# Performance work log

Hardware: AMD Instinct MI355X
Metric: run time of the kernel (lower is better)

The kernel has to match this reference:

```python
import jax, jax.numpy as jnp
import numpy as np

N, C, D = 16384, 1000, 512


def setup_inputs() -> dict:
    key = jax.random.key(0)
    k1, k2, k3 = jax.random.split(key, 3)
    features = jax.random.normal(k1, (N, D), dtype=jnp.float32)
    centers = jax.random.uniform(k2, (C, D), dtype=jnp.float32)  # torch.rand init
    labels = jax.random.randint(k3, (N,), 0, C, dtype=jnp.int64)
    return {"features": features, "centers": centers, "labels": labels}


def reference(features, centers, labels):
    # Full N x C squared Euclidean distance matrix (as in torch.cdist(...)**2)
    f2 = jnp.sum(features * features, axis=1, keepdims=True)      # [N,1]
    c2 = jnp.sum(centers * centers, axis=1)[None, :]               # [1,C]
    d2 = f2 + c2 - 2.0 * (features @ centers.T)                    # [N,C]
    # Select the distance to each sample's own class center
    sel = jnp.take_along_axis(d2, labels[:, None].astype(jnp.int32), axis=1)[:, 0]  # [N]
    sel = jnp.clip(sel, 1e-12, 1e12)
    return jnp.mean(sel)
```

## Files before the change

kernel.cpp:

```cpp
#include <hip/hip_runtime.h>


typedef float f32x4 __attribute__((ext_vector_type(4)));

#define CL_BLOCKS 2048
#define CL_WAVES  (CL_BLOCKS * 4)

__global__ __launch_bounds__(256) void cl_stage1_partial(
    const float* __restrict__ feat,
    const float* __restrict__ cent,
    const int* __restrict__ labels,
    float* __restrict__ partial,
    int N) {
  const int lane = threadIdx.x & 63;
  const int wave = blockIdx.x * 4 + (threadIdx.x >> 6);

  const f32x4* __restrict__ fp4 = reinterpret_cast<const f32x4*>(feat);
  const f32x4* __restrict__ cp4 = reinterpret_cast<const f32x4*>(cent);

  const int n0 = wave;
  const int n1 = wave + CL_WAVES;

  float acc = 0.0f;

  if (n1 < N) {
    const int l0 = labels[n0];
    const int l1 = labels[n1];
    const size_t f0 = (size_t)n0 * 128 + lane;
    const size_t f1 = (size_t)n1 * 128 + lane;
    const size_t c0 = (size_t)l0 * 128 + lane;
    const size_t c1 = (size_t)l1 * 128 + lane;

    const f32x4 a0 = __builtin_nontemporal_load(&fp4[f0]);
    const f32x4 a1 = __builtin_nontemporal_load(&fp4[f0 + 64]);
    const f32x4 a2 = __builtin_nontemporal_load(&fp4[f1]);
    const f32x4 a3 = __builtin_nontemporal_load(&fp4[f1 + 64]);
    const f32x4 b0 = cp4[c0];
    const f32x4 b1 = cp4[c0 + 64];
    const f32x4 b2 = cp4[c1];
    const f32x4 b3 = cp4[c1 + 64];

    f32x4 d;
    d = a0 - b0; acc += d.x * d.x + d.y * d.y + d.z * d.z + d.w * d.w;
    d = a1 - b1; acc += d.x * d.x + d.y * d.y + d.z * d.z + d.w * d.w;
    d = a2 - b2; acc += d.x * d.x + d.y * d.y + d.z * d.z + d.w * d.w;
    d = a3 - b3; acc += d.x * d.x + d.y * d.y + d.z * d.z + d.w * d.w;
  } else if (n0 < N) {
    const int l0 = labels[n0];
    const size_t f0 = (size_t)n0 * 128 + lane;
    const size_t c0 = (size_t)l0 * 128 + lane;
    const f32x4 a0 = __builtin_nontemporal_load(&fp4[f0]);
    const f32x4 a1 = __builtin_nontemporal_load(&fp4[f0 + 64]);
    const f32x4 b0 = cp4[c0];
    const f32x4 b1 = cp4[c0 + 64];
    f32x4 d;
    d = a0 - b0; acc += d.x * d.x + d.y * d.y + d.z * d.z + d.w * d.w;
    d = a1 - b1; acc += d.x * d.x + d.y * d.y + d.z * d.z + d.w * d.w;
  }

#pragma unroll
  for (int off = 32; off; off >>= 1) acc += __shfl_xor(acc, off, 64);

  if (lane == 0) partial[wave] = acc;
}

__global__ __launch_bounds__(256) void cl_stage2_reduce(
    const float* __restrict__ partial,
    float* __restrict__ out, float invN) {
  const int lane = threadIdx.x & 63;
  const int wid  = threadIdx.x >> 6;

  const f32x4* __restrict__ p4 = reinterpret_cast<const f32x4*>(partial);
  float acc = 0.0f;
#pragma unroll
  for (int j = 0; j < CL_WAVES / 4 / 256; ++j) {
    const f32x4 v = p4[threadIdx.x + j * 256];
    acc += v.x + v.y + v.z + v.w;
  }

#pragma unroll
  for (int off = 32; off; off >>= 1) acc += __shfl_xor(acc, off, 64);

  __shared__ float wave_sums[4];
  if (lane == 0) wave_sums[wid] = acc;
  __syncthreads();
  if (threadIdx.x == 0) {
    out[0] = (wave_sums[0] + wave_sums[1] + wave_sums[2] + wave_sums[3]) * invN;
  }
}

extern "C" void kernel_launch(void* const* d_in, const int* in_sizes, int n_in,
                              void* d_out, int out_size, void* d_ws, size_t ws_size,
                              hipStream_t stream) {
  const float* feat   = (const float*)d_in[0];
  const float* cent   = (const float*)d_in[1];
  const int*   labels = (const int*)d_in[2];
  float*       out    = (float*)d_out;
  float*       parts  = (float*)d_ws;

  const int N = in_sizes[2];

  cl_stage1_partial<<<CL_BLOCKS, 256, 0, stream>>>(feat, cent, labels, parts, N);
  cl_stage2_reduce<<<1, 256, 0, stream>>>(parts, out, 1.0f / (float)N);
}
```

Before: 13.48 us.

## Fuse reduction into main kernel via grouped atomics and last-block finalize

Replaces the two-kernel partial-sum-then-reduce scheme with a single kernel where each block atomically adds its sum into one of 32 group accumulators, and a two-level atomic counter identifies the last block, which sums the groups and writes the mean. This removes the second kernel launch and the partial buffer round-trip. In exchange it adds a memset launch on the workspace, atomic contention, and a memory-ordering dependence that rests on device-scope atomics rather than an explicit fence.

```diff
diff --git a/kernel.cpp b/kernel.cpp
--- a/kernel.cpp
+++ b/kernel.cpp
@@ -5,15 +5,20 @@
 
 #define CL_BLOCKS 2048
 #define CL_WAVES  (CL_BLOCKS * 4)
+#define NGRP      32
+#define BPG       (CL_BLOCKS / NGRP)
 
-__global__ __launch_bounds__(256) void cl_stage1_partial(
+__global__ __launch_bounds__(256) void cl_fused(
     const float* __restrict__ feat,
     const float* __restrict__ cent,
     const int* __restrict__ labels,
-    float* __restrict__ partial,
-    int N) {
+    float* __restrict__ gacc,
+    unsigned int* __restrict__ cnt,
+    float* __restrict__ out,
+    int N, float invN) {
   const int lane = threadIdx.x & 63;
-  const int wave = blockIdx.x * 4 + (threadIdx.x >> 6);
+  const int wid  = threadIdx.x >> 6;
+  const int wave = blockIdx.x * 4 + wid;
 
   const f32x4* __restrict__ fp4 = reinterpret_cast<const f32x4*>(feat);
   const f32x4* __restrict__ cp4 = reinterpret_cast<const f32x4*>(cent);
@@ -61,31 +66,35 @@
 #pragma unroll
   for (int off = 32; off; off >>= 1) acc += __shfl_xor(acc, off, 64);
 
-  if (lane == 0) partial[wave] = acc;
-}
+  __shared__ float wsum[4];
+  __shared__ int is_final;
+  if (lane == 0) wsum[wid] = acc;
+  __syncthreads();
 
-__global__ __launch_bounds__(256) void cl_stage2_reduce(
-    const float* __restrict__ partial,
-    float* __restrict__ out, float invN) {
-  const int lane = threadIdx.x & 63;
-  const int wid  = threadIdx.x >> 6;
+  if (threadIdx.x == 0) {
+    const float bs = wsum[0] + wsum[1] + wsum[2] + wsum[3];
+    const int g = blockIdx.x & (NGRP - 1);
 
-  const f32x4* __restrict__ p4 = reinterpret_cast<const f32x4*>(partial);
-  float acc = 0.0f;
+    const float old = atomicAdd(&gacc[g], bs);
+    asm volatile("" :: "v"(old) : "memory");
+
+    int last = 0;
+    const unsigned r = atomicAdd(&cnt[g], 1u);
+    if (r == BPG - 1u) {
+      const unsigned r2 = atomicAdd(&cnt[NGRP], 1u);
+      last = (r2 == NGRP - 1u);
+    }
+    is_final = last;
+  }
+  __syncthreads();
+  if (!is_final) return;
+
+  float v = 0.0f;
+  if (threadIdx.x < NGRP) v = atomicAdd(&gacc[threadIdx.x], 0.0f);
+  if (threadIdx.x < 64) {
 #pragma unroll
-  for (int j = 0; j < CL_WAVES / 4 / 256; ++j) {
-    const f32x4 v = p4[threadIdx.x + j * 256];
-    acc += v.x + v.y + v.z + v.w;
-  }
-
-#pragma unroll
-  for (int off = 32; off; off >>= 1) acc += __shfl_xor(acc, off, 64);
-
-  __shared__ float wave_sums[4];
-  if (lane == 0) wave_sums[wid] = acc;
-  __syncthreads();
-  if (threadIdx.x == 0) {
-    out[0] = (wave_sums[0] + wave_sums[1] + wave_sums[2] + wave_sums[3]) * invN;
+    for (int off = 32; off; off >>= 1) v += __shfl_xor(v, off, 64);
+    if (threadIdx.x == 0) out[0] = v * invN;
   }
 }
 
@@ -96,10 +105,14 @@
   const float* cent   = (const float*)d_in[1];
   const int*   labels = (const int*)d_in[2];
   float*       out    = (float*)d_out;
-  float*       parts  = (float*)d_ws;
+
+  float*        gacc = (float*)d_ws;
+  unsigned int* cnt  = (unsigned int*)((char*)d_ws + NGRP * 4);
 
   const int N = in_sizes[2];
 
-  cl_stage1_partial<<<CL_BLOCKS, 256, 0, stream>>>(feat, cent, labels, parts, N);
-  cl_stage2_reduce<<<1, 256, 0, stream>>>(parts, out, 1.0f / (float)N);
+  hipMemsetAsync(d_ws, 0, (2 * NGRP + 1) * 4, stream);
+
+  cl_fused<<<CL_BLOCKS, 256, 0, stream>>>(feat, cent, labels, gacc, cnt, out,
+                                          N, 1.0f / (float)N);
 }
```

Result: slower. 37.35 us (+177.1%).
